# Kernel tuning notes

Measured on AMD Instinct MI355X. Metric: run time of the kernel, lower is better.

## Reference

```python
import jax, jax.numpy as jnp
import numpy as np

N_NODES = 165888   # 2048 puzzles * 81 cells
N_EDGES = 3317760  # 2048 * 1620 directed sudoku-constraint edges
HID = 64
N_LAYERS = 4
LN_EPS = 1e-5


def setup_inputs() -> dict:
    key = jax.random.key(0)
    ks = jax.random.split(key, 16)
    x = jax.random.normal(ks[0], (N_NODES, 9), dtype=jnp.float32)
    edge_index = jax.random.randint(ks[1], (2, N_EDGES), 0, N_NODES, dtype=jnp.int64)
    s = 0.1
    return {
        "x": x,
        "edge_index": edge_index,
        "W_in": jax.random.normal(ks[2], (HID, 9), dtype=jnp.float32) * s,
        "b_in": jnp.zeros((HID,), jnp.float32),
        "W_rel": jax.random.normal(ks[3], (N_LAYERS, HID, HID), dtype=jnp.float32) * s,
        "W_root": jax.random.normal(ks[4], (N_LAYERS, HID, HID), dtype=jnp.float32) * s,
        "b_conv": jnp.zeros((N_LAYERS, HID), jnp.float32),
        "W_res": jax.random.normal(ks[5], (HID, HID), dtype=jnp.float32) * s,
        "b_res": jnp.zeros((HID,), jnp.float32),
        "ln_g": jnp.ones((HID,), jnp.float32),
        "ln_b": jnp.zeros((HID,), jnp.float32),
        "W_out": jax.random.normal(ks[6], (9, HID), dtype=jnp.float32) * s,
        "b_out": jnp.zeros((9,), jnp.float32),
    }


def _layer_norm(h, g, b):
    mu = jnp.mean(h, axis=-1, keepdims=True)
    var = jnp.mean(jnp.square(h - mu), axis=-1, keepdims=True)
    return (h - mu) * jax.lax.rsqrt(var + LN_EPS) * g + b


def reference(x, edge_index, W_in, b_in, W_rel, W_root, b_conv, W_res, b_res,
              ln_g, ln_b, W_out, b_out):
    # input projection: [N, 9] -> [N, HID]
    h = x @ W_in.T + b_in
    residual = h @ W_res.T + b_res  # computed once before the conv stack
    src, dst = edge_index[0], edge_index[1]
    n = h.shape[0]
    for l in range(N_LAYERS):
        # GraphConv (PyG semantics, aggr='add'): gather neighbor feats, scatter-add to dst
        agg = jax.ops.segment_sum(h[src], dst, num_segments=n)
        h = h @ W_root[l].T + agg @ W_rel[l].T + b_conv[l]
        h = _layer_norm(h, ln_g, ln_b)
        h = jnp.where(h > 0, h, 0.01 * h)  # leaky_relu(0.01); dropout = identity (eval)
        h = h + residual
    out = h @ W_out.T + b_out  # [N, 9]
    return out.reshape(-1, 9, 9, 9)
```

## Files before the change

### kernel.cpp

```cpp
#include <hip/hip_runtime.h>

#define N_NODES 165888
#define N_EDGES 3317760
#define NBKT 648
#define NB 512
#define EPB (N_EDGES / NB)
#define HSZ (NBKT * NB)
#define LN_EPS 1e-5f

typedef _Float16 f16;
typedef _Float16 half8 __attribute__((ext_vector_type(8)));
typedef float f32x4 __attribute__((ext_vector_type(4)));

__device__ __forceinline__ f32x4 mfma16(half8 a, half8 b, f32x4 c) {
    return __builtin_amdgcn_mfma_f32_16x16x32_f16(a, b, c, 0, 0, 0);
}


__global__ __launch_bounds__(256) void k_hist2d(const int* __restrict__ dst,
                                                int* __restrict__ h2) {
    __shared__ int hist[NBKT];
    int t = threadIdx.x, b = blockIdx.x;
    for (int i = t; i < NBKT; i += 256) hist[i] = 0;
    __syncthreads();
    int e0 = b * EPB;
    for (int e = e0 + t; e < e0 + EPB; e += 256)
        atomicAdd(&hist[dst[e] >> 8], 1);
    __syncthreads();
    for (int i = t; i < NBKT; i += 256)
        h2[i * NB + b] = hist[i];
}

__global__ void k_scan1(int* __restrict__ h2, int* __restrict__ bsum) {
    __shared__ int s[1024];
    int t = threadIdx.x;
    int i = blockIdx.x * 1024 + t;
    int own = h2[i];
    s[t] = own;
    __syncthreads();
    for (int off = 1; off < 1024; off <<= 1) {
        int u = (t >= off) ? s[t - off] : 0;
        __syncthreads();
        s[t] += u;
        __syncthreads();
    }
    h2[i] = s[t] - own;
    if (t == 1023) bsum[blockIdx.x] = s[1023];
}

__global__ void k_scan2(const int* __restrict__ bsum, int* __restrict__ bsumx,
                        int* __restrict__ h2) {
    __shared__ int s[512];
    int t = threadIdx.x;
    int v = (t < HSZ / 1024) ? bsum[t] : 0;
    s[t] = v;
    __syncthreads();
    for (int off = 1; off < 512; off <<= 1) {
        int u = (t >= off) ? s[t - off] : 0;
        __syncthreads();
        s[t] += u;
        __syncthreads();
    }
    if (t < HSZ / 1024) bsumx[t] = s[t] - v;
    if (t == 0) h2[HSZ] = N_EDGES;
}

__global__ void k_scan3(int* __restrict__ h2, const int* __restrict__ bsumx) {
    int i = blockIdx.x * 1024 + threadIdx.x;
    h2[i] += bsumx[blockIdx.x];
}

__global__ __launch_bounds__(256) void k_scatter(const int* __restrict__ src,
                                                 const int* __restrict__ dst,
                                                 const int* __restrict__ h2,
                                                 unsigned* __restrict__ pairs) {
    __shared__ int cur[NBKT];
    int t = threadIdx.x, b = blockIdx.x;
    for (int i = t; i < NBKT; i += 256) cur[i] = h2[i * NB + b];
    __syncthreads();
    int e0 = b * EPB;
    for (int e = e0 + t; e < e0 + EPB; e += 256) {
        int d = dst[e];
        int pos = atomicAdd(&cur[d >> 8], 1);
        pairs[pos] = ((unsigned)(d & 255) << 24) | (unsigned)src[e];
    }
}

__global__ __launch_bounds__(256) void k_csr(const unsigned* __restrict__ pairs,
                                             const int* __restrict__ h2,
                                             int* __restrict__ roff,
                                             int* __restrict__ csr) {
    __shared__ int hist[256];
    __shared__ int sc[256];
    __shared__ int curs[256];
    int b = blockIdx.x;
    int e0 = h2[b * NB], e1 = h2[(b + 1) * NB];
    int t = threadIdx.x;
    hist[t] = 0;
    __syncthreads();
    for (int p = e0 + t; p < e1; p += 256)
        atomicAdd(&hist[pairs[p] >> 24], 1);
    __syncthreads();
    int own = hist[t];
    sc[t] = own;
    __syncthreads();
    for (int off = 1; off < 256; off <<= 1) {
        int u = (t >= off) ? sc[t - off] : 0;
        __syncthreads();
        sc[t] += u;
        __syncthreads();
    }
    int base = e0 + sc[t] - own;
    roff[(b << 8) + t] = base;
    curs[t] = base;
    if (b == 0 && t == 0) roff[N_NODES] = N_EDGES;
    __syncthreads();
    for (int p = e0 + t; p < e1; p += 256) {
        unsigned pk = pairs[p];
        int pos = atomicAdd(&curs[pk >> 24], 1);
        csr[pos] = (int)(pk & 0xFFFFFF);
    }
}


__global__ void k_wcvt(const float* __restrict__ Wroot, const float* __restrict__ Wrel,
                       const float* __restrict__ Wres, const float* __restrict__ Win,
                       f16* __restrict__ W2h, f16* __restrict__ Wresh, f16* __restrict__ Winh) {
    int i = blockIdx.x * 256 + threadIdx.x;
    if (i < 4 * 64 * 128) {
        int l = i >> 13, r = i & 8191, j = r >> 7, k = r & 127;
        float v = (k < 64) ? Wroot[l * 4096 + j * 64 + k] : Wrel[l * 4096 + j * 64 + k - 64];
        W2h[i] = (f16)v;
    } else if (i < 4 * 64 * 128 + 4096) {
        int t = i - 4 * 64 * 128;
        Wresh[t] = (f16)Wres[t];
    } else if (i < 4 * 64 * 128 + 4096 + 2048) {
        int t = i - (4 * 64 * 128 + 4096);
        int j = t >> 5, k = t & 31;
        Winh[t] = (k < 9) ? (f16)Win[j * 9 + k] : (f16)0.f;
    }
}


__global__ __launch_bounds__(256) void k_proj(
        const float* __restrict__ x, const f16* __restrict__ Winh,
        const float* __restrict__ bin, const f16* __restrict__ Wresh,
        const float* __restrict__ bres, f16* __restrict__ h0,
        f16* __restrict__ res) {
    __shared__ f16 hs[4][16][64];
    int tid = threadIdx.x, w = tid >> 6, lane = tid & 63, li = lane & 15, kg = lane >> 4;
    int nb = blockIdx.x * 64 + w * 16;
    int node = nb + li;

    half8 ax;
    #pragma unroll
    for (int e = 0; e < 8; ++e) ax[e] = (f16)0.f;
    if (kg == 0) {
        #pragma unroll
        for (int e = 0; e < 8; ++e) ax[e] = (f16)x[(size_t)node * 9 + e];
    } else if (kg == 1) {
        ax[0] = (f16)x[(size_t)node * 9 + 8];
    }

    f32x4 ch[4];
    #pragma unroll
    for (int jt = 0; jt < 4; ++jt) {
        half8 b = *(const half8*)(Winh + (jt * 16 + li) * 32 + kg * 8);
        f32x4 z = {0.f, 0.f, 0.f, 0.f};
        ch[jt] = mfma16(ax, b, z);
    }
    #pragma unroll
    for (int jt = 0; jt < 4; ++jt) {
        float bb = bin[jt * 16 + li];
        #pragma unroll
        for (int r = 0; r < 4; ++r) {
            int row = kg * 4 + r;
            float v = ch[jt][r] + bb;
            f16 hv = (f16)v;
            h0[(size_t)(nb + row) * 64 + jt * 16 + li] = hv;
            int col = jt * 16 + li;
            hs[w][row][col ^ ((row & 7) * 8)] = hv;
        }
    }
    __syncthreads();

    f32x4 cr[4];
    #pragma unroll
    for (int jt = 0; jt < 4; ++jt) { f32x4 z = {0.f,0.f,0.f,0.f}; cr[jt] = z; }
    #pragma unroll
    for (int s = 0; s < 2; ++s) {
        int k0 = s * 32 + kg * 8;
        half8 a = *(const half8*)(&hs[w][li][k0 ^ ((li & 7) * 8)]);
        #pragma unroll
        for (int jt = 0; jt < 4; ++jt) {
            half8 b = *(const half8*)(Wresh + (jt * 16 + li) * 64 + k0);
            cr[jt] = mfma16(a, b, cr[jt]);
        }
    }
    #pragma unroll
    for (int jt = 0; jt < 4; ++jt) {
        float bb = bres[jt * 16 + li];
        #pragma unroll
        for (int r = 0; r < 4; ++r)
            res[(size_t)(nb + kg * 4 + r) * 64 + jt * 16 + li] = (f16)(cr[jt][r] + bb);
    }
}


__global__ __launch_bounds__(256) void k_gather(
        const f16* __restrict__ h, const int* __restrict__ roff,
        const int* __restrict__ csr, f16* __restrict__ agg) {
    int lane = threadIdx.x & 63;
    int gwave = (blockIdx.x * blockDim.x + threadIdx.x) >> 6;
    int nw = (gridDim.x * blockDim.x) >> 6;
    int g = lane >> 3, s = lane & 7;
    for (int n = gwave; n < N_NODES; n += nw) {
        int e0 = roff[n], e1 = roff[n + 1];
        float a0 = 0, a1 = 0, a2 = 0, a3 = 0, a4 = 0, a5 = 0, a6 = 0, a7 = 0;
        int p = e0 + g;
        for (; p + 8 < e1; p += 16) {
            int i0 = csr[p];
            int i1 = csr[p + 8];
            half8 v0 = *(const half8*)(h + ((size_t)i0 << 6) + s * 8);
            half8 v1 = *(const half8*)(h + ((size_t)i1 << 6) + s * 8);
            a0 += (float)v0[0] + (float)v1[0];
            a1 += (float)v0[1] + (float)v1[1];
            a2 += (float)v0[2] + (float)v1[2];
            a3 += (float)v0[3] + (float)v1[3];
            a4 += (float)v0[4] + (float)v1[4];
            a5 += (float)v0[5] + (float)v1[5];
            a6 += (float)v0[6] + (float)v1[6];
            a7 += (float)v0[7] + (float)v1[7];
        }
        if (p < e1) {
            int i0 = csr[p];
            half8 v0 = *(const half8*)(h + ((size_t)i0 << 6) + s * 8);
            a0 += (float)v0[0]; a1 += (float)v0[1];
            a2 += (float)v0[2]; a3 += (float)v0[3];
            a4 += (float)v0[4]; a5 += (float)v0[5];
            a6 += (float)v0[6]; a7 += (float)v0[7];
        }
        #pragma unroll
        for (int off = 8; off <= 32; off <<= 1) {
            a0 += __shfl_xor(a0, off, 64);
            a1 += __shfl_xor(a1, off, 64);
            a2 += __shfl_xor(a2, off, 64);
            a3 += __shfl_xor(a3, off, 64);
            a4 += __shfl_xor(a4, off, 64);
            a5 += __shfl_xor(a5, off, 64);
            a6 += __shfl_xor(a6, off, 64);
            a7 += __shfl_xor(a7, off, 64);
        }
        if (lane < 8) {
            half8 o;
            o[0] = (f16)a0; o[1] = (f16)a1; o[2] = (f16)a2; o[3] = (f16)a3;
            o[4] = (f16)a4; o[5] = (f16)a5; o[6] = (f16)a6; o[7] = (f16)a7;
            *(half8*)(agg + ((size_t)n << 6) + s * 8) = o;
        }
    }
}


__global__ __launch_bounds__(256) void k_update(
        const f16* __restrict__ h, const f16* __restrict__ agg,
        const f16* __restrict__ res, const f16* __restrict__ W2h,
        const float* __restrict__ bconv, const float* __restrict__ lng,
        const float* __restrict__ lnb, f16* __restrict__ hn) {
    int tid = threadIdx.x, w = tid >> 6, lane = tid & 63, li = lane & 15, kg = lane >> 4;
    int nb = blockIdx.x * 64 + w * 16;
    int node = nb + li;

    f32x4 acc[4];
    #pragma unroll
    for (int jt = 0; jt < 4; ++jt) { f32x4 z = {0.f,0.f,0.f,0.f}; acc[jt] = z; }

    #pragma unroll
    for (int s = 0; s < 4; ++s) {
        half8 a = (s < 2)
            ? *(const half8*)(h   + ((size_t)node << 6) + s * 32 + kg * 8)
            : *(const half8*)(agg + ((size_t)node << 6) + (s - 2) * 32 + kg * 8);
        #pragma unroll
        for (int jt = 0; jt < 4; ++jt) {
            half8 b = *(const half8*)(W2h + (size_t)(jt * 16 + li) * 128 + s * 32 + kg * 8);
            acc[jt] = mfma16(a, b, acc[jt]);
        }
    }

    #pragma unroll
    for (int jt = 0; jt < 4; ++jt) {
        float bb = bconv[jt * 16 + li];
        #pragma unroll
        for (int r = 0; r < 4; ++r) acc[jt][r] += bb;
    }

    float mu[4], rstd[4];
    #pragma unroll
    for (int r = 0; r < 4; ++r) {
        float v = acc[0][r] + acc[1][r] + acc[2][r] + acc[3][r];
        v += __shfl_xor(v, 1, 64); v += __shfl_xor(v, 2, 64);
        v += __shfl_xor(v, 4, 64); v += __shfl_xor(v, 8, 64);
        mu[r] = v * (1.f / 64.f);
    }
    #pragma unroll
    for (int r = 0; r < 4; ++r) {
        float d0 = acc[0][r] - mu[r], d1 = acc[1][r] - mu[r];
        float d2 = acc[2][r] - mu[r], d3 = acc[3][r] - mu[r];
        float vv = d0 * d0 + d1 * d1 + d2 * d2 + d3 * d3;
        vv += __shfl_xor(vv, 1, 64); vv += __shfl_xor(vv, 2, 64);
        vv += __shfl_xor(vv, 4, 64); vv += __shfl_xor(vv, 8, 64);
        rstd[r] = rsqrtf(vv * (1.f / 64.f) + LN_EPS);
    }
    #pragma unroll
    for (int jt = 0; jt < 4; ++jt) {
        float gg = lng[jt * 16 + li], bb = lnb[jt * 16 + li];
        #pragma unroll
        for (int r = 0; r < 4; ++r) {
            float y = (acc[jt][r] - mu[r]) * rstd[r] * gg + bb;
            y = (y > 0.f) ? y : 0.01f * y;
            y += (float)res[(size_t)(nb + kg * 4 + r) * 64 + jt * 16 + li];
            hn[(size_t)(nb + kg * 4 + r) * 64 + jt * 16 + li] = (f16)y;
        }
    }
}


__global__ __launch_bounds__(256) void k_out(
        const f16* __restrict__ h, const float* __restrict__ Wout,
        const float* __restrict__ bout, float* __restrict__ out) {
    int node = blockIdx.x * 256 + threadIdx.x;
    float acc[9];
    #pragma unroll
    for (int c = 0; c < 9; ++c) acc[c] = bout[c];
    #pragma unroll
    for (int cc = 0; cc < 8; ++cc) {
        half8 v = *(const half8*)(h + ((size_t)node << 6) + cc * 8);
        float f[8];
        #pragma unroll
        for (int e = 0; e < 8; ++e) f[e] = (float)v[e];
        #pragma unroll
        for (int c = 0; c < 9; ++c) {
            #pragma unroll
            for (int e = 0; e < 8; ++e)
                acc[c] += f[e] * Wout[c * 64 + cc * 8 + e];
        }
    }
    #pragma unroll
    for (int c = 0; c < 9; ++c) out[(size_t)node * 9 + c] = acc[c];
}

extern "C" void kernel_launch(void* const* d_in, const int* in_sizes, int n_in,
                              void* d_out, int out_size, void* d_ws, size_t ws_size,
                              hipStream_t stream) {
    const float* x     = (const float*)d_in[0];
    const int*   ei    = (const int*)d_in[1];
    const float* Win   = (const float*)d_in[2];
    const float* bin   = (const float*)d_in[3];
    const float* Wrel  = (const float*)d_in[4];
    const float* Wroot = (const float*)d_in[5];
    const float* bconv = (const float*)d_in[6];
    const float* Wres  = (const float*)d_in[7];
    const float* bres  = (const float*)d_in[8];
    const float* lng   = (const float*)d_in[9];
    const float* lnb   = (const float*)d_in[10];
    const float* Wout  = (const float*)d_in[11];
    const float* bout  = (const float*)d_in[12];
    float* out = (float*)d_out;

    char* p = (char*)d_ws;
    auto alloc = [&](size_t bytes) {
        char* r = p;
        p += (bytes + 255) & ~(size_t)255;
        return r;
    };
    f16*      h0    = (f16*)alloc((size_t)N_NODES * 64 * 2);
    f16*      h1    = (f16*)alloc((size_t)N_NODES * 64 * 2);
    f16*      res   = (f16*)alloc((size_t)N_NODES * 64 * 2);
    f16*      agg   = (f16*)alloc((size_t)N_NODES * 64 * 2);
    unsigned* pairs = (unsigned*)alloc((size_t)N_EDGES * 4);
    int*      csr   = (int*)alloc((size_t)N_EDGES * 4);
    int*      roff  = (int*)alloc((size_t)(N_NODES + 1) * 4);
    int*      h2    = (int*)alloc((size_t)(HSZ + 1) * 4);
    int*      bsum  = (int*)alloc((HSZ / 1024) * 4);
    int*      bsumx = (int*)alloc((HSZ / 1024) * 4);
    f16*      W2h   = (f16*)alloc(4 * 64 * 128 * 2);
    f16*      Wresh = (f16*)alloc(64 * 64 * 2);
    f16*      Winh  = (f16*)alloc(64 * 32 * 2);

    const int* srcv = ei;
    const int* dstv = ei + N_EDGES;

    k_hist2d<<<NB, 256, 0, stream>>>(dstv, h2);
    k_scan1<<<HSZ / 1024, 1024, 0, stream>>>(h2, bsum);
    k_scan2<<<1, 512, 0, stream>>>(bsum, bsumx, h2);
    k_scan3<<<HSZ / 1024, 1024, 0, stream>>>(h2, bsumx);
    k_scatter<<<NB, 256, 0, stream>>>(srcv, dstv, h2, pairs);
    k_csr<<<NBKT, 256, 0, stream>>>(pairs, h2, roff, csr);

    k_wcvt<<<152, 256, 0, stream>>>(Wroot, Wrel, Wres, Win, W2h, Wresh, Winh);
    k_proj<<<N_NODES / 64, 256, 0, stream>>>(x, Winh, bin, Wresh, bres, h0, res);

    f16* ha = h0;
    f16* hb = h1;
    for (int l = 0; l < 4; ++l) {
        k_gather<<<4096, 256, 0, stream>>>(ha, roff, csr, agg);
        k_update<<<N_NODES / 64, 256, 0, stream>>>(ha, agg, res, W2h + (size_t)l * 64 * 128,
                                                   bconv + l * 64, lng, lnb, hb);
        f16* t = ha; ha = hb; hb = t;
    }
    k_out<<<N_NODES / 256, 256, 0, stream>>>(ha, Wout, bout, out);
}
```

Measured before the change: 501.5 us.

## Fuse neighbor gather with per-layer GEMM and LayerNorm update kernel

Merges the separate gather and update kernels into one per-layer kernel. Each wave aggregates neighbors for 16 nodes into a swizzled shared-memory tile, then feeds that tile straight into the MFMA update, so the agg buffer is no longer written to and read back from global memory. The gather mapping also changes: 8 lanes now handle one node serially with a 4-way unrolled edge loop, replacing 64 lanes per node with a shuffle reduction. This removes one launch and the agg traffic per layer, but gives each lane a longer serial gather chain and may change load balance and memory-level parallelism.

```diff
diff --git a/kernel.cpp b/kernel.cpp
--- a/kernel.cpp
+++ b/kernel.cpp
@@ -207,32 +207,40 @@
 }
 
 
-__global__ __launch_bounds__(256) void k_gather(
-        const f16* __restrict__ h, const int* __restrict__ roff,
-        const int* __restrict__ csr, f16* __restrict__ agg) {
-    int lane = threadIdx.x & 63;
-    int gwave = (blockIdx.x * blockDim.x + threadIdx.x) >> 6;
-    int nw = (gridDim.x * blockDim.x) >> 6;
+__global__ __launch_bounds__(256) void k_layer(
+        const f16* __restrict__ h, const f16* __restrict__ res,
+        const int* __restrict__ roff, const int* __restrict__ csr,
+        const f16* __restrict__ W2h, const float* __restrict__ bconv,
+        const float* __restrict__ lng, const float* __restrict__ lnb,
+        f16* __restrict__ hn) {
+    __shared__ f16 hs[4][16][64];
+    int tid = threadIdx.x, lane = tid & 63, w = tid >> 6;
     int g = lane >> 3, s = lane & 7;
-    for (int n = gwave; n < N_NODES; n += nw) {
+    int blk = blockIdx.x;
+
+    #pragma unroll
+    for (int r2 = 0; r2 < 2; ++r2) {
+        int nl = r2 * 8 + g;
+        int n = blk * 64 + w * 16 + nl;
         int e0 = roff[n], e1 = roff[n + 1];
         float a0 = 0, a1 = 0, a2 = 0, a3 = 0, a4 = 0, a5 = 0, a6 = 0, a7 = 0;
-        int p = e0 + g;
-        for (; p + 8 < e1; p += 16) {
-            int i0 = csr[p];
-            int i1 = csr[p + 8];
+        int p = e0;
+        for (; p + 3 < e1; p += 4) {
+            int i0 = csr[p], i1 = csr[p + 1], i2 = csr[p + 2], i3 = csr[p + 3];
             half8 v0 = *(const half8*)(h + ((size_t)i0 << 6) + s * 8);
             half8 v1 = *(const half8*)(h + ((size_t)i1 << 6) + s * 8);
-            a0 += (float)v0[0] + (float)v1[0];
-            a1 += (float)v0[1] + (float)v1[1];
-            a2 += (float)v0[2] + (float)v1[2];
-            a3 += (float)v0[3] + (float)v1[3];
-            a4 += (float)v0[4] + (float)v1[4];
-            a5 += (float)v0[5] + (float)v1[5];
-            a6 += (float)v0[6] + (float)v1[6];
-            a7 += (float)v0[7] + (float)v1[7];
-        }
-        if (p < e1) {
+            half8 v2 = *(const half8*)(h + ((size_t)i2 << 6) + s * 8);
+            half8 v3 = *(const half8*)(h + ((size_t)i3 << 6) + s * 8);
+            a0 += ((float)v0[0] + (float)v1[0]) + ((float)v2[0] + (float)v3[0]);
+            a1 += ((float)v0[1] + (float)v1[1]) + ((float)v2[1] + (float)v3[1]);
+            a2 += ((float)v0[2] + (float)v1[2]) + ((float)v2[2] + (float)v3[2]);
+            a3 += ((float)v0[3] + (float)v1[3]) + ((float)v2[3] + (float)v3[3]);
+            a4 += ((float)v0[4] + (float)v1[4]) + ((float)v2[4] + (float)v3[4]);
+            a5 += ((float)v0[5] + (float)v1[5]) + ((float)v2[5] + (float)v3[5]);
+            a6 += ((float)v0[6] + (float)v1[6]) + ((float)v2[6] + (float)v3[6]);
+            a7 += ((float)v0[7] + (float)v1[7]) + ((float)v2[7] + (float)v3[7]);
+        }
+        for (; p < e1; ++p) {
             int i0 = csr[p];
             half8 v0 = *(const half8*)(h + ((size_t)i0 << 6) + s * 8);
             a0 += (float)v0[0]; a1 += (float)v0[1];
@@ -240,49 +248,33 @@
             a4 += (float)v0[4]; a5 += (float)v0[5];
             a6 += (float)v0[6]; a7 += (float)v0[7];
         }
-        #pragma unroll
-        for (int off = 8; off <= 32; off <<= 1) {
-            a0 += __shfl_xor(a0, off, 64);
-            a1 += __shfl_xor(a1, off, 64);
-            a2 += __shfl_xor(a2, off, 64);
-            a3 += __shfl_xor(a3, off, 64);
-            a4 += __shfl_xor(a4, off, 64);
-            a5 += __shfl_xor(a5, off, 64);
-            a6 += __shfl_xor(a6, off, 64);
-            a7 += __shfl_xor(a7, off, 64);
-        }
-        if (lane < 8) {
-            half8 o;
-            o[0] = (f16)a0; o[1] = (f16)a1; o[2] = (f16)a2; o[3] = (f16)a3;
-            o[4] = (f16)a4; o[5] = (f16)a5; o[6] = (f16)a6; o[7] = (f16)a7;
-            *(half8*)(agg + ((size_t)n << 6) + s * 8) = o;
-        }
-    }
-}
-
-
-__global__ __launch_bounds__(256) void k_update(
-        const f16* __restrict__ h, const f16* __restrict__ agg,
-        const f16* __restrict__ res, const f16* __restrict__ W2h,
-        const float* __restrict__ bconv, const float* __restrict__ lng,
-        const float* __restrict__ lnb, f16* __restrict__ hn) {
-    int tid = threadIdx.x, w = tid >> 6, lane = tid & 63, li = lane & 15, kg = lane >> 4;
-    int nb = blockIdx.x * 64 + w * 16;
+        half8 o;
+        o[0] = (f16)a0; o[1] = (f16)a1; o[2] = (f16)a2; o[3] = (f16)a3;
+        o[4] = (f16)a4; o[5] = (f16)a5; o[6] = (f16)a6; o[7] = (f16)a7;
+        *(half8*)(&hs[w][nl][(s ^ (nl & 7)) * 8]) = o;
+    }
+
+    int li = lane & 15, kg = lane >> 4;
+    int nb = blk * 64 + w * 16;
     int node = nb + li;
 
-    f32x4 acc[4];
-    #pragma unroll
-    for (int jt = 0; jt < 4; ++jt) { f32x4 z = {0.f,0.f,0.f,0.f}; acc[jt] = z; }
-
-    #pragma unroll
-    for (int s = 0; s < 4; ++s) {
-        half8 a = (s < 2)
-            ? *(const half8*)(h   + ((size_t)node << 6) + s * 32 + kg * 8)
-            : *(const half8*)(agg + ((size_t)node << 6) + (s - 2) * 32 + kg * 8);
+    f32x4 C[4];
+    #pragma unroll
+    for (int jt = 0; jt < 4; ++jt) { f32x4 z = {0.f,0.f,0.f,0.f}; C[jt] = z; }
+
+    #pragma unroll
+    for (int st = 0; st < 4; ++st) {
+        half8 a;
+        if (st < 2) {
+            a = *(const half8*)(h + ((size_t)node << 6) + st * 32 + kg * 8);
+        } else {
+            int m = (st - 2) * 4 + kg;
+            a = *(const half8*)(&hs[w][li][(m ^ (li & 7)) * 8]);
+        }
         #pragma unroll
         for (int jt = 0; jt < 4; ++jt) {
-            half8 b = *(const half8*)(W2h + (size_t)(jt * 16 + li) * 128 + s * 32 + kg * 8);
-            acc[jt] = mfma16(a, b, acc[jt]);
+            half8 b = *(const half8*)(W2h + (size_t)(jt * 16 + li) * 128 + st * 32 + kg * 8);
+            C[jt] = mfma16(a, b, C[jt]);
         }
     }
 
@@ -290,21 +282,21 @@
     for (int jt = 0; jt < 4; ++jt) {
         float bb = bconv[jt * 16 + li];
         #pragma unroll
-        for (int r = 0; r < 4; ++r) acc[jt][r] += bb;
+        for (int r = 0; r < 4; ++r) C[jt][r] += bb;
     }
 
     float mu[4], rstd[4];
     #pragma unroll
     for (int r = 0; r < 4; ++r) {
-        float v = acc[0][r] + acc[1][r] + acc[2][r] + acc[3][r];
+        float v = C[0][r] + C[1][r] + C[2][r] + C[3][r];
         v += __shfl_xor(v, 1, 64); v += __shfl_xor(v, 2, 64);
         v += __shfl_xor(v, 4, 64); v += __shfl_xor(v, 8, 64);
         mu[r] = v * (1.f / 64.f);
     }
     #pragma unroll
     for (int r = 0; r < 4; ++r) {
-        float d0 = acc[0][r] - mu[r], d1 = acc[1][r] - mu[r];
-        float d2 = acc[2][r] - mu[r], d3 = acc[3][r] - mu[r];
+        float d0 = C[0][r] - mu[r], d1 = C[1][r] - mu[r];
+        float d2 = C[2][r] - mu[r], d3 = C[3][r] - mu[r];
         float vv = d0 * d0 + d1 * d1 + d2 * d2 + d3 * d3;
         vv += __shfl_xor(vv, 1, 64); vv += __shfl_xor(vv, 2, 64);
         vv += __shfl_xor(vv, 4, 64); vv += __shfl_xor(vv, 8, 64);
@@ -315,10 +307,11 @@
         float gg = lng[jt * 16 + li], bb = lnb[jt * 16 + li];
         #pragma unroll
         for (int r = 0; r < 4; ++r) {
-            float y = (acc[jt][r] - mu[r]) * rstd[r] * gg + bb;
+            size_t idx = (size_t)(nb + kg * 4 + r) * 64 + jt * 16 + li;
+            float y = (C[jt][r] - mu[r]) * rstd[r] * gg + bb;
             y = (y > 0.f) ? y : 0.01f * y;
-            y += (float)res[(size_t)(nb + kg * 4 + r) * 64 + jt * 16 + li];
-            hn[(size_t)(nb + kg * 4 + r) * 64 + jt * 16 + li] = (f16)y;
+            y += (float)res[idx];
+            hn[idx] = (f16)y;
         }
     }
 }
@@ -375,7 +368,6 @@
     f16*      h0    = (f16*)alloc((size_t)N_NODES * 64 * 2);
     f16*      h1    = (f16*)alloc((size_t)N_NODES * 64 * 2);
     f16*      res   = (f16*)alloc((size_t)N_NODES * 64 * 2);
-    f16*      agg   = (f16*)alloc((size_t)N_NODES * 64 * 2);
     unsigned* pairs = (unsigned*)alloc((size_t)N_EDGES * 4);
     int*      csr   = (int*)alloc((size_t)N_EDGES * 4);
     int*      roff  = (int*)alloc((size_t)(N_NODES + 1) * 4);
@@ -402,9 +394,9 @@
     f16* ha = h0;
     f16* hb = h1;
     for (int l = 0; l < 4; ++l) {
-        k_gather<<<4096, 256, 0, stream>>>(ha, roff, csr, agg);
-        k_update<<<N_NODES / 64, 256, 0, stream>>>(ha, agg, res, W2h + (size_t)l * 64 * 128,
-                                                   bconv + l * 64, lng, lnb, hb);
+        k_layer<<<N_NODES / 64, 256, 0, stream>>>(ha, res, roff, csr,
+                                                  W2h + (size_t)l * 64 * 128,
+                                                  bconv + l * 64, lng, lnb, hb);
         f16* t = ha; ha = hb; hb = t;
     }
     k_out<<<N_NODES / 256, 256, 0, stream>>>(ha, Wout, bout, out);
```

New measurement: 456.3 us. -9.0%, faster.
